# Optimization experiments

Measured on AMD Instinct MI355X. Metric: run time of the kernel, lower is better.

## Reference

```python
import jax, jax.numpy as jnp
import numpy as np

B, N, E, H = 2, 512, 128, 256
IN_DIM = 3 * E + 1


def setup_inputs() -> dict:
    key = jax.random.key(0)
    ks = jax.random.split(key, 9)
    node_embed = jax.random.normal(ks[0], (B, N, E), dtype=jnp.float32)
    problems = jax.random.uniform(ks[1], (B, N, 4), dtype=jnp.float32)
    euclid = jax.random.uniform(ks[2], (B, N, N), dtype=jnp.float32)
    euclid = 0.5 * (euclid + jnp.swapaxes(euclid, 1, 2))  # symmetric, realistic
    s = 0.02
    W1 = s * jax.random.normal(ks[3], (IN_DIM, H), dtype=jnp.float32)
    b1 = jnp.zeros((H,), jnp.float32)
    W2 = s * jax.random.normal(ks[4], (H, H), dtype=jnp.float32)
    b2 = jnp.zeros((H,), jnp.float32)
    W3 = s * jax.random.normal(ks[5], (H, 1), dtype=jnp.float32)
    b3 = jnp.zeros((1,), jnp.float32)
    return {"node_embed": node_embed, "problems": problems,
            "euclid_distance_matrix": euclid,
            "W1": W1, "b1": b1, "W2": W2, "b2": b2, "W3": W3, "b3": b3}


def _forward(node_embed, euclid, W1, b1, W2, b2, W3, b3):
    b, n, e = node_embed.shape
    hi = jnp.broadcast_to(node_embed[:, :, None, :], (b, n, n, e))
    hj = jnp.broadcast_to(node_embed[:, None, :, :], (b, n, n, e))
    habs = jnp.abs(node_embed[:, :, None, :] - node_embed[:, None, :, :])
    x = jnp.concatenate([hi, hj, habs, euclid[..., None]], axis=-1)  # (B,N,N,3E+1)
    h = jax.nn.relu(jnp.einsum('bijf,fh->bijh', x, W1) + b1)
    h = jax.nn.relu(jnp.einsum('bijh,hg->bijg', h, W2) + b2)
    pred = (jnp.einsum('bijh,ho->bijo', h, W3) + b3)[..., 0]  # (B,N,N)
    pred = 0.5 * (pred + jnp.swapaxes(pred, 1, 2))
    pred = pred * (1.0 - jnp.eye(n, dtype=pred.dtype))  # zero diagonal
    return pred


def reference(node_embed, problems, euclid_distance_matrix, W1, b1, W2, b2, W3, b3):
    # euclid_distance_matrix provided, so `problems` fallback path is unused
    return _forward(node_embed, euclid_distance_matrix, W1, b1, W2, b2, W3, b3)
```

## Files before the change

### kernel.cpp

```cpp
#include <hip/hip_runtime.h>
#include <hip/hip_bf16.h>


#define BN 512
#define EE 128
#define HH 256

typedef __attribute__((ext_vector_type(8)))  short short8;
typedef __attribute__((ext_vector_type(4)))  short short4v;
typedef __attribute__((ext_vector_type(16))) float f32x16;
typedef __attribute__((ext_vector_type(4)))  float f32x4;

static __device__ __forceinline__ unsigned short f2bf(float f) {
    __bf16 h = (__bf16)f;
    return __builtin_bit_cast(unsigned short, h);
}
static __device__ __forceinline__ f32x16 zero16() {
    f32x16 v;
    #pragma unroll
    for (int i = 0; i < 16; ++i) v[i] = 0.f;
    return v;
}
#define MFMA(a, b, c) __builtin_amdgcn_mfma_f32_32x32x16_bf16((a), (b), (c), 0, 0, 0)

__global__ void prep(const float* __restrict__ node, const float* __restrict__ W1,
                     const float* __restrict__ W2, const float* __restrict__ b1,
                     float* __restrict__ PA,
                     unsigned short* __restrict__ w1c_p, unsigned short* __restrict__ w1b_p,
                     unsigned short* __restrict__ w2_p,  unsigned short* __restrict__ w1d_f) {
    int blk = blockIdx.x;
    if (blk < 256) {
        int idx = blk * 256 + threadIdx.x;
        {
            int t = idx & 7, l = (idx >> 3) & 63, mt = (idx >> 9) & 7, kb = idx >> 12;
            int k = kb * 16 + (l >> 5) * 8 + t, m = mt * 32 + (l & 31);
            w2_p[idx] = f2bf(W2[k * HH + m]);
            if (idx < 32768) {
                w1c_p[idx] = f2bf(W1[(2 * EE + k) * HH + m]);
                w1b_p[idx] = f2bf(W1[(EE + k) * HH + m]);
            }
        }
        if (idx < 4096) {
            int t = idx & 7, l = (idx >> 3) & 63, mt = idx >> 9;
            int m = mt * 32 + (l & 31);
            bool nz = (t == 0 && l < 32);
            w1d_f[idx] = nz ? f2bf(W1[(3 * EE) * HH + m]) : (unsigned short)0;
        }
    } else {
        int bi = blk - 256;
        int h = threadIdx.x;
        const float* nd = node + (size_t)bi * EE;
        float sa = b1[h];
        #pragma unroll 8
        for (int e = 0; e < EE; ++e) sa += nd[e] * W1[e * HH + h];
        PA[bi * HH + h] = sa;
    }
}

__global__ __launch_bounds__(256, 2) void edge_main(
    const float* __restrict__ node, const float* __restrict__ euclid,
    const float* __restrict__ W3, const float* __restrict__ b3,
    const float* __restrict__ b2v, const float* __restrict__ PA,
    const unsigned short* __restrict__ w1c_p, const unsigned short* __restrict__ w1b_p,
    const unsigned short* __restrict__ w2_p,  const unsigned short* __restrict__ w1d_f,
    float* __restrict__ out)
{
    __shared__ __align__(16) unsigned short lds_buf[2 * 128 * 136];
    __shared__ float pp[512];

    const int jt = blockIdx.x, i = blockIdx.y, b = blockIdx.z;
    const int jbase = jt * 128;
    const int tid = threadIdx.x, wave = tid >> 6, lane = tid & 63;
    const int m0 = lane & 31, q = lane >> 5;

    unsigned short* ldsD  = lds_buf;
    unsigned short* ldsHJ = lds_buf + 128 * 136;
    unsigned short* ldsH1 = lds_buf;

    {
        int row = tid >> 1, half = tid & 1;
        const f32x4* nj = (const f32x4*)(node + ((size_t)b * BN + jbase + row) * EE);
        const f32x4* hv = (const f32x4*)(node + ((size_t)b * BN + i) * EE);
        #pragma unroll
        for (int g = 0; g < 8; ++g) {
            int c0 = half * 16 + g * 2;
            f32x4 a0 = nj[c0], a1 = nj[c0 + 1];
            f32x4 h0 = hv[c0], h1v = hv[c0 + 1];
            short8 pd, ph;
            #pragma unroll
            for (int u = 0; u < 4; ++u) {
                pd[u]     = (short)f2bf(fabsf(a0[u] - h0[u]));
                pd[4 + u] = (short)f2bf(fabsf(a1[u] - h1v[u]));
                ph[u]     = (short)f2bf(a0[u]);
                ph[4 + u] = (short)f2bf(a1[u]);
            }
            int off = row * 136 + half * 64 + g * 8;
            *(short8*)&ldsD[off]  = pd;
            *(short8*)&ldsHJ[off] = ph;
        }
    }
    __syncthreads();

    f32x16 acc[2][4];
    #pragma unroll
    for (int mt = 0; mt < 2; ++mt)
        #pragma unroll
        for (int nt = 0; nt < 4; ++nt) acc[mt][nt] = zero16();
    {
        const short8* wc = (const short8*)w1c_p;
        const short8* wb = (const short8*)w1b_p;
        const int mtg = wave * 2;
        #pragma unroll
        for (int kb = 0; kb < 8; ++kb) {
            short8 ac0 = wc[(kb * 8 + mtg + 0) * 64 + lane];
            short8 ac1 = wc[(kb * 8 + mtg + 1) * 64 + lane];
            short8 ab0 = wb[(kb * 8 + mtg + 0) * 64 + lane];
            short8 ab1 = wb[(kb * 8 + mtg + 1) * 64 + lane];
            #pragma unroll
            for (int nt = 0; nt < 4; ++nt) {
                int off = (nt * 32 + m0) * 136 + kb * 16 + q * 8;
                short8 bD  = *(const short8*)&ldsD[off];
                short8 bHJ = *(const short8*)&ldsHJ[off];
                acc[0][nt] = MFMA(ac0, bD, acc[0][nt]);
                acc[1][nt] = MFMA(ac1, bD, acc[1][nt]);
                acc[0][nt] = MFMA(ab0, bHJ, acc[0][nt]);
                acc[1][nt] = MFMA(ab1, bHJ, acc[1][nt]);
            }
        }
        const float* erow = euclid + ((size_t)b * BN + i) * BN + jbase;
        short8 aw0 = ((const short8*)w1d_f)[(mtg + 0) * 64 + lane];
        short8 aw1 = ((const short8*)w1d_f)[(mtg + 1) * 64 + lane];
        #pragma unroll
        for (int nt = 0; nt < 4; ++nt) {
            short8 be;
            #pragma unroll
            for (int u = 0; u < 8; ++u) be[u] = 0;
            if (lane < 32) be[0] = (short)f2bf(erow[nt * 32 + m0]);
            acc[0][nt] = MFMA(aw0, be, acc[0][nt]);
            acc[1][nt] = MFMA(aw1, be, acc[1][nt]);
        }
    }
    __syncthreads();

    {
        const float* paB = PA + ((size_t)b * BN + i) * HH;
        #pragma unroll
        for (int mt = 0; mt < 2; ++mt) {
            #pragma unroll
            for (int rg = 0; rg < 4; ++rg) {
                int f0 = wave * 64 + mt * 32 + rg * 8;
                f32x4 plo = *(const f32x4*)&paB[f0];
                f32x4 phi = *(const f32x4*)&paB[f0 + 4];
                f32x4 pav;
                #pragma unroll
                for (int u = 0; u < 4; ++u) pav[u] = q ? phi[u] : plo[u];
                #pragma unroll
                for (int nt = 0; nt < 4; ++nt) {
                    short4v w;
                    #pragma unroll
                    for (int u = 0; u < 4; ++u) {
                        float v = acc[mt][nt][rg * 4 + u] + pav[u];
                        v = v > 0.f ? v : 0.f;
                        w[u] = (short)f2bf(v);
                    }
                    *(short4v*)&ldsH1[(nt * 32 + m0) * 264 + f0 + 4 * q] = w;
                }
            }
        }
    }
    __syncthreads();

    f32x16 c2[2][4];
    #pragma unroll
    for (int mt = 0; mt < 2; ++mt)
        #pragma unroll
        for (int nt = 0; nt < 4; ++nt) c2[mt][nt] = zero16();
    {
        const short8* w2f = (const short8*)w2_p;
        const int mtg = wave * 2;
        #pragma unroll
        for (int kb = 0; kb < 16; ++kb) {
            short8 a0 = w2f[(kb * 8 + mtg + 0) * 64 + lane];
            short8 a1 = w2f[(kb * 8 + mtg + 1) * 64 + lane];
            #pragma unroll
            for (int nt = 0; nt < 4; ++nt) {
                short8 bh = *(const short8*)&ldsH1[(nt * 32 + m0) * 264 + kb * 16 + q * 8];
                c2[0][nt] = MFMA(a0, bh, c2[0][nt]);
                c2[1][nt] = MFMA(a1, bh, c2[1][nt]);
            }
        }
    }

    {
        float s[4] = {0.f, 0.f, 0.f, 0.f};
        #pragma unroll
        for (int mt = 0; mt < 2; ++mt) {
            #pragma unroll
            for (int rg = 0; rg < 4; ++rg) {
                int f0 = wave * 64 + mt * 32 + rg * 8;
                f32x4 blo = *(const f32x4*)&b2v[f0];
                f32x4 bhi = *(const f32x4*)&b2v[f0 + 4];
                f32x4 wlo = *(const f32x4*)&W3[f0];
                f32x4 whi = *(const f32x4*)&W3[f0 + 4];
                #pragma unroll
                for (int u = 0; u < 4; ++u) {
                    float bb = q ? bhi[u] : blo[u];
                    float ww = q ? whi[u] : wlo[u];
                    #pragma unroll
                    for (int nt = 0; nt < 4; ++nt) {
                        float h2 = c2[mt][nt][rg * 4 + u] + bb;
                        h2 = h2 > 0.f ? h2 : 0.f;
                        s[nt] += h2 * ww;
                    }
                }
            }
        }
        #pragma unroll
        for (int nt = 0; nt < 4; ++nt)
            s[nt] += __shfl_xor(s[nt], 32, 64);
        if (lane < 32) {
            #pragma unroll
            for (int nt = 0; nt < 4; ++nt)
                pp[wave * 128 + nt * 32 + lane] = s[nt];
        }
    }
    __syncthreads();
    if (tid < 128) {
        float v = pp[tid] + pp[128 + tid] + pp[256 + tid] + pp[384 + tid] + b3[0];
        out[((size_t)b * BN + i) * BN + jbase + tid] = v;
    }
}

__global__ void symmetrize(float* __restrict__ out) {
    int b = blockIdx.z, ti = blockIdx.y, tj = blockIdx.x;
    if (tj < ti) return;
    int i = ti * 32 + threadIdx.y, j = tj * 32 + threadIdx.x;
    float* p = out + (size_t)b * BN * BN;
    if (i == j) { p[(size_t)i * BN + j] = 0.f; return; }
    if (j < i) return;
    float a = p[(size_t)i * BN + j];
    float c = p[(size_t)j * BN + i];
    float v = 0.5f * (a + c);
    p[(size_t)i * BN + j] = v;
    p[(size_t)j * BN + i] = v;
}

extern "C" void kernel_launch(void* const* d_in, const int* in_sizes, int n_in,
                              void* d_out, int out_size, void* d_ws, size_t ws_size,
                              hipStream_t stream) {
    const float* node   = (const float*)d_in[0];
    const float* euclid = (const float*)d_in[2];
    const float* W1     = (const float*)d_in[3];
    const float* b1     = (const float*)d_in[4];
    const float* W2     = (const float*)d_in[5];
    const float* b2     = (const float*)d_in[6];
    const float* W3     = (const float*)d_in[7];
    const float* b3     = (const float*)d_in[8];
    float* out = (float*)d_out;

    char* ws = (char*)d_ws;
    float*          PA    = (float*)ws;
    unsigned short* w1c_p = (unsigned short*)(ws + (1u << 20));
    unsigned short* w1b_p = (unsigned short*)(ws + (1u << 20) + 65536);
    unsigned short* w2_p  = (unsigned short*)(ws + (1u << 20) + 131072);
    unsigned short* w1d_f = (unsigned short*)(ws + (1u << 20) + 262144);

    prep<<<1280, 256, 0, stream>>>(node, W1, W2, b1, PA, w1c_p, w1b_p, w2_p, w1d_f);
    edge_main<<<dim3(BN / 128, BN, 2), 256, 0, stream>>>(
        node, euclid, W3, b3, b2, PA, w1c_p, w1b_p, w2_p, w1d_f, out);
    symmetrize<<<dim3(BN / 32, BN / 32, 2), dim3(32, 32), 0, stream>>>(out);
}
```

Baseline: 235.9 us.

## Precompute hj projection per node and fold euclid term into epilogue

The hj·W1b contribution depends only on node j, so prep now computes a per-node projection PB and the edge kernel adds it in the epilogue instead of running MFMAs over an hj tile. The euclid column is applied as a scalar FMA with the fp32 W1 row rather than a mostly-zero MFMA. This halves the layer-1 MFMA work and removes the hj LDS tile. In exchange the epilogue reads PB rows from global memory for each element group, which adds memory traffic and latency.

```diff
diff --git a/kernel.cpp b/kernel.cpp
--- a/kernel.cpp
+++ b/kernel.cpp
@@ -25,47 +25,41 @@
 
 __global__ void prep(const float* __restrict__ node, const float* __restrict__ W1,
                      const float* __restrict__ W2, const float* __restrict__ b1,
-                     float* __restrict__ PA,
-                     unsigned short* __restrict__ w1c_p, unsigned short* __restrict__ w1b_p,
-                     unsigned short* __restrict__ w2_p,  unsigned short* __restrict__ w1d_f) {
+                     float* __restrict__ PA, float* __restrict__ PB,
+                     unsigned short* __restrict__ w1c_p, unsigned short* __restrict__ w2_p) {
     int blk = blockIdx.x;
     if (blk < 256) {
         int idx = blk * 256 + threadIdx.x;
-        {
-            int t = idx & 7, l = (idx >> 3) & 63, mt = (idx >> 9) & 7, kb = idx >> 12;
-            int k = kb * 16 + (l >> 5) * 8 + t, m = mt * 32 + (l & 31);
-            w2_p[idx] = f2bf(W2[k * HH + m]);
-            if (idx < 32768) {
-                w1c_p[idx] = f2bf(W1[(2 * EE + k) * HH + m]);
-                w1b_p[idx] = f2bf(W1[(EE + k) * HH + m]);
-            }
-        }
-        if (idx < 4096) {
-            int t = idx & 7, l = (idx >> 3) & 63, mt = idx >> 9;
-            int m = mt * 32 + (l & 31);
-            bool nz = (t == 0 && l < 32);
-            w1d_f[idx] = nz ? f2bf(W1[(3 * EE) * HH + m]) : (unsigned short)0;
-        }
+        int t = idx & 7, l = (idx >> 3) & 63, mt = (idx >> 9) & 7, kb = idx >> 12;
+        int k = kb * 16 + (l >> 5) * 8 + t, m = mt * 32 + (l & 31);
+        w2_p[idx] = f2bf(W2[k * HH + m]);
+        if (idx < 32768)
+            w1c_p[idx] = f2bf(W1[(2 * EE + k) * HH + m]);
     } else {
         int bi = blk - 256;
         int h = threadIdx.x;
         const float* nd = node + (size_t)bi * EE;
-        float sa = b1[h];
+        float sa = b1[h], sb = 0.f;
         #pragma unroll 8
-        for (int e = 0; e < EE; ++e) sa += nd[e] * W1[e * HH + h];
+        for (int e = 0; e < EE; ++e) {
+            float nv = nd[e];
+            sa += nv * W1[e * HH + h];
+            sb += nv * W1[(EE + e) * HH + h];
+        }
         PA[bi * HH + h] = sa;
+        PB[bi * HH + h] = sb;
     }
 }
 
 __global__ __launch_bounds__(256, 2) void edge_main(
     const float* __restrict__ node, const float* __restrict__ euclid,
-    const float* __restrict__ W3, const float* __restrict__ b3,
-    const float* __restrict__ b2v, const float* __restrict__ PA,
-    const unsigned short* __restrict__ w1c_p, const unsigned short* __restrict__ w1b_p,
-    const unsigned short* __restrict__ w2_p,  const unsigned short* __restrict__ w1d_f,
+    const float* __restrict__ W1, const float* __restrict__ W3,
+    const float* __restrict__ b3, const float* __restrict__ b2v,
+    const float* __restrict__ PA, const float* __restrict__ PB,
+    const unsigned short* __restrict__ w1c_p, const unsigned short* __restrict__ w2_p,
     float* __restrict__ out)
 {
-    __shared__ __align__(16) unsigned short lds_buf[2 * 128 * 136];
+    __shared__ __align__(16) unsigned short lds_buf[128 * 264];
     __shared__ float pp[512];
 
     const int jt = blockIdx.x, i = blockIdx.y, b = blockIdx.z;
@@ -74,7 +68,6 @@
     const int m0 = lane & 31, q = lane >> 5;
 
     unsigned short* ldsD  = lds_buf;
-    unsigned short* ldsHJ = lds_buf + 128 * 136;
     unsigned short* ldsH1 = lds_buf;
 
     {
@@ -86,17 +79,13 @@
             int c0 = half * 16 + g * 2;
             f32x4 a0 = nj[c0], a1 = nj[c0 + 1];
             f32x4 h0 = hv[c0], h1v = hv[c0 + 1];
-            short8 pd, ph;
+            short8 pd;
             #pragma unroll
             for (int u = 0; u < 4; ++u) {
                 pd[u]     = (short)f2bf(fabsf(a0[u] - h0[u]));
                 pd[4 + u] = (short)f2bf(fabsf(a1[u] - h1v[u]));
-                ph[u]     = (short)f2bf(a0[u]);
-                ph[4 + u] = (short)f2bf(a1[u]);
-            }
-            int off = row * 136 + half * 64 + g * 8;
-            *(short8*)&ldsD[off]  = pd;
-            *(short8*)&ldsHJ[off] = ph;
+            }
+            *(short8*)&ldsD[row * 136 + half * 64 + g * 8] = pd;
         }
     }
     __syncthreads();
@@ -108,42 +97,29 @@
         for (int nt = 0; nt < 4; ++nt) acc[mt][nt] = zero16();
     {
         const short8* wc = (const short8*)w1c_p;
-        const short8* wb = (const short8*)w1b_p;
         const int mtg = wave * 2;
         #pragma unroll
         for (int kb = 0; kb < 8; ++kb) {
             short8 ac0 = wc[(kb * 8 + mtg + 0) * 64 + lane];
             short8 ac1 = wc[(kb * 8 + mtg + 1) * 64 + lane];
-            short8 ab0 = wb[(kb * 8 + mtg + 0) * 64 + lane];
-            short8 ab1 = wb[(kb * 8 + mtg + 1) * 64 + lane];
             #pragma unroll
             for (int nt = 0; nt < 4; ++nt) {
-                int off = (nt * 32 + m0) * 136 + kb * 16 + q * 8;
-                short8 bD  = *(const short8*)&ldsD[off];
-                short8 bHJ = *(const short8*)&ldsHJ[off];
+                short8 bD = *(const short8*)&ldsD[(nt * 32 + m0) * 136 + kb * 16 + q * 8];
                 acc[0][nt] = MFMA(ac0, bD, acc[0][nt]);
                 acc[1][nt] = MFMA(ac1, bD, acc[1][nt]);
-                acc[0][nt] = MFMA(ab0, bHJ, acc[0][nt]);
-                acc[1][nt] = MFMA(ab1, bHJ, acc[1][nt]);
-            }
-        }
+            }
+        }
+    }
+    __syncthreads();
+
+    {
+        const float* paB  = PA + ((size_t)b * BN + i) * HH;
+        const float* pbB  = PB + ((size_t)b * BN + jbase) * HH;
+        const float* wd   = W1 + (size_t)(3 * EE) * HH;
         const float* erow = euclid + ((size_t)b * BN + i) * BN + jbase;
-        short8 aw0 = ((const short8*)w1d_f)[(mtg + 0) * 64 + lane];
-        short8 aw1 = ((const short8*)w1d_f)[(mtg + 1) * 64 + lane];
-        #pragma unroll
-        for (int nt = 0; nt < 4; ++nt) {
-            short8 be;
-            #pragma unroll
-            for (int u = 0; u < 8; ++u) be[u] = 0;
-            if (lane < 32) be[0] = (short)f2bf(erow[nt * 32 + m0]);
-            acc[0][nt] = MFMA(aw0, be, acc[0][nt]);
-            acc[1][nt] = MFMA(aw1, be, acc[1][nt]);
-        }
-    }
-    __syncthreads();
-
-    {
-        const float* paB = PA + ((size_t)b * BN + i) * HH;
+        float ev[4];
+        #pragma unroll
+        for (int nt = 0; nt < 4; ++nt) ev[nt] = erow[nt * 32 + m0];
         #pragma unroll
         for (int mt = 0; mt < 2; ++mt) {
             #pragma unroll
@@ -151,15 +127,21 @@
                 int f0 = wave * 64 + mt * 32 + rg * 8;
                 f32x4 plo = *(const f32x4*)&paB[f0];
                 f32x4 phi = *(const f32x4*)&paB[f0 + 4];
-                f32x4 pav;
+                f32x4 dlo = *(const f32x4*)&wd[f0];
+                f32x4 dhi = *(const f32x4*)&wd[f0 + 4];
+                f32x4 pav, wdv;
                 #pragma unroll
-                for (int u = 0; u < 4; ++u) pav[u] = q ? phi[u] : plo[u];
+                for (int u = 0; u < 4; ++u) {
+                    pav[u] = q ? phi[u] : plo[u];
+                    wdv[u] = q ? dhi[u] : dlo[u];
+                }
                 #pragma unroll
                 for (int nt = 0; nt < 4; ++nt) {
+                    f32x4 pbv = *(const f32x4*)&pbB[(size_t)(nt * 32 + m0) * HH + f0 + 4 * q];
                     short4v w;
                     #pragma unroll
                     for (int u = 0; u < 4; ++u) {
-                        float v = acc[mt][nt][rg * 4 + u] + pav[u];
+                        float v = acc[mt][nt][rg * 4 + u] + pav[u] + pbv[u] + ev[nt] * wdv[u];
                         v = v > 0.f ? v : 0.f;
                         w[u] = (short)f2bf(v);
                     }
@@ -260,13 +242,12 @@
 
     char* ws = (char*)d_ws;
     float*          PA    = (float*)ws;
-    unsigned short* w1c_p = (unsigned short*)(ws + (1u << 20));
-    unsigned short* w1b_p = (unsigned short*)(ws + (1u << 20) + 65536);
-    unsigned short* w2_p  = (unsigned short*)(ws + (1u << 20) + 131072);
-    unsigned short* w1d_f = (unsigned short*)(ws + (1u << 20) + 262144);
-
-    prep<<<1280, 256, 0, stream>>>(node, W1, W2, b1, PA, w1c_p, w1b_p, w2_p, w1d_f);
+    float*          PB    = (float*)(ws + (1u << 20));
+    unsigned short* w1c_p = (unsigned short*)(ws + (2u << 20));
+    unsigned short* w2_p  = (unsigned short*)(ws + (2u << 20) + 65536);
+
+    prep<<<1280, 256, 0, stream>>>(node, W1, W2, b1, PA, PB, w1c_p, w2_p);
     edge_main<<<dim3(BN / 128, BN, 2), 256, 0, stream>>>(
-        node, euclid, W3, b3, b2, PA, w1c_p, w1b_p, w2_p, w1d_f, out);
+        node, euclid, W1, W3, b3, b2, PA, PB, w1c_p, w2_p, out);
     symmetrize<<<dim3(BN / 32, BN / 32, 2), dim3(32, 32), 0, stream>>>(out);
 }
```

Result: slower. 266.8 us (+13.1%).
